# Performance work log

Measured on AMD Instinct MI355X. Metric: run time of the kernel, lower is better.

Reference implementation:

```python
import jax, jax.numpy as jnp
import numpy as np


def _cdist(x, y):
    # x: (b, n, c), y: (b, m, c) -> (b, n, m) Euclidean distances
    x2 = jnp.sum(x * x, axis=-1, keepdims=True)          # (b, n, 1)
    y2 = jnp.sum(y * y, axis=-1)[:, None, :]             # (b, 1, m)
    xy = jnp.einsum('bnc,bmc->bnm', x, y)                # (b, n, m)
    d2 = jnp.maximum(x2 + y2 - 2.0 * xy, 0.0)
    return jnp.sqrt(d2)


def setup_inputs() -> dict:
    key = jax.random.key(0)
    k1, k2, k3, k4 = jax.random.split(key, 4)
    bs, N, M, C = 8, 4096, 4096, 128
    return {
        'set1': jax.random.normal(k1, (bs, N, C), dtype=jnp.float32),
        'set2': jax.random.normal(k2, (bs, M, C), dtype=jnp.float32),
        'w1': jax.random.uniform(k3, (bs, N), dtype=jnp.float32),
        'w2': jax.random.uniform(k4, (bs, M), dtype=jnp.float32),
    }


def reference(set1, set2, w1, w2):
    dist = _cdist(set1, set2)                 # (b, N, M)
    out_dist = jnp.min(dist, axis=2)          # (b, N)
    out_dist2 = jnp.min(dist, axis=1)         # (b, M)
    total = (jnp.sum(w1 * out_dist) + jnp.sum(w2 * out_dist2)) / 2.0
    return total
```

## Files before the change

### kernel.cpp

```cpp
#include <hip/hip_runtime.h>

#define BS 8
#define NN 4096
#define MM 4096
#define CC 128
#define XT 128
#define YT 64
#define MH 2048
#define NYT (MH / YT)
#define NXT (NN / XT)

#define FINF_BITS 0x7F800000u

typedef __attribute__((ext_vector_type(8))) short bf16x8;
typedef __attribute__((ext_vector_type(4))) float f32x4;

__device__ inline ushort f2bf(float f) {
    unsigned u = __float_as_uint(f);
    unsigned r = (u + 0x7FFFu + ((u >> 16) & 1u)) >> 16;
    return (ushort)r;
}

__global__ void ch_prep(const float* __restrict__ y,
                        ushort* __restrict__ y16, float* __restrict__ yn,
                        unsigned* __restrict__ rowmin, unsigned* __restrict__ colmin,
                        float* __restrict__ out) {
    int gid = blockIdx.x * blockDim.x + threadIdx.x;
    size_t i = (size_t)gid * 4;

    float4 w = *(const float4*)(y + i);
    ushort4 p;
    p.x = f2bf(w.x); p.y = f2bf(w.y); p.z = f2bf(w.z); p.w = f2bf(w.w);
    *(ushort4*)(y16 + i) = p;
    float sy = w.x * w.x + w.y * w.y + w.z * w.z + w.w * w.w;

#pragma unroll
    for (int mask = 1; mask <= 16; mask <<= 1)
        sy += __shfl_xor(sy, mask, 64);
    if ((threadIdx.x & 31) == 0)
        yn[gid >> 5] = sy;

    if (gid < BS * NN) rowmin[gid] = FINF_BITS;
    if (gid < BS * MM) colmin[gid] = FINF_BITS;
    if (gid == 0) out[0] = 0.0f;
}

__global__ __launch_bounds__(256) void ch_tile(
    const float* __restrict__ Xf, const ushort* __restrict__ Y,
    const float* __restrict__ yn,
    unsigned* __restrict__ rowmin, unsigned* __restrict__ colmin) {

    __shared__ ushort xs[XT * CC];
    __shared__ ushort ys[2][YT * CC];
    __shared__ unsigned coltile[MH];
    __shared__ unsigned rowtile[XT];
    __shared__ float xnorm[XT];

    const int b  = blockIdx.x;
    const int xt = blockIdx.y;
    const int mh = blockIdx.z;
    const int n0 = xt * XT;
    const int m0 = mh * MH;
    const int tid  = threadIdx.x;
    const int wave = tid >> 6;
    const int lane = tid & 63;
    const int lc   = lane & 15;
    const int quad = lane >> 4;
    const int wm = wave >> 1;
    const int wn = wave & 1;

    const ushort* Yb = Y + ((size_t)b * MM + m0) * CC;

    const float* Xb = Xf + ((size_t)b * NN + n0) * CC;
    {
        float psum[8];
#pragma unroll
        for (int s = 0; s < 8; ++s) {
            int flat = s * 256 + tid;
            int r = flat >> 4, c = flat & 15;
            float4 v0 = *(const float4*)(Xb + (size_t)r * CC + c * 8);
            float4 v1 = *(const float4*)(Xb + (size_t)r * CC + c * 8 + 4);
            ushort h[8] = {f2bf(v0.x), f2bf(v0.y), f2bf(v0.z), f2bf(v0.w),
                           f2bf(v1.x), f2bf(v1.y), f2bf(v1.z), f2bf(v1.w)};
            *(bf16x8*)(xs + r * CC + (c ^ (r & 7)) * 8) = *(bf16x8*)h;
            psum[s] = v0.x * v0.x + v0.y * v0.y + v0.z * v0.z + v0.w * v0.w +
                      v1.x * v1.x + v1.y * v1.y + v1.z * v1.z + v1.w * v1.w;
        }
#pragma unroll
        for (int mask = 1; mask <= 8; mask <<= 1)
#pragma unroll
            for (int s = 0; s < 8; ++s)
                psum[s] += __shfl_xor(psum[s], mask, 64);
        if ((tid & 15) == 0) {
#pragma unroll
            for (int s = 0; s < 8; ++s)
                xnorm[s * 16 + (tid >> 4)] = psum[s];
        }
    }
    for (int c2 = tid; c2 < MH; c2 += 256) coltile[c2] = FINF_BITS;
    if (tid < XT) rowtile[tid] = FINF_BITS;

#pragma unroll
    for (int s = 0; s < 4; ++s) {
        int f = s * 256 + tid;
        int r = f >> 4, c = f & 15;
        const ushort* g = Yb + (size_t)r * CC + (c ^ (r & 15)) * 8;
        ushort* l = ys[0] + (s * 256 + wave * 64) * 8;
        __builtin_amdgcn_global_load_lds(
            (const __attribute__((address_space(1))) void*)g,
            (__attribute__((address_space(3))) void*)l, 16, 0, 0);
    }

    __syncthreads();

    float xnp[4][4];
#pragma unroll
    for (int i = 0; i < 4; ++i) {
        float4 t = *(const float4*)(&xnorm[wm * 64 + i * 16 + quad * 4]);
        xnp[i][0] = t.x; xnp[i][1] = t.y; xnp[i][2] = t.z; xnp[i][3] = t.w;
    }
    float rm[4][4];
#pragma unroll
    for (int i = 0; i < 4; ++i)
#pragma unroll
        for (int r = 0; r < 4; ++r) rm[i][r] = __builtin_inff();

    const float* ynb = yn + (size_t)b * MM + m0;
    const int xrow = (wm * 64 + lc) * CC;
    const int yrow = (wn * 32 + lc) * CC;
    const int xsw  = lc & 7;

#pragma unroll 1
    for (int mt = 0; mt < NYT; ++mt) {
        if (mt) __syncthreads();

        if (mt + 1 < NYT) {
            const ushort* Ysrc = Yb + (size_t)(mt + 1) * YT * CC;
            ushort* dstb = ys[(mt + 1) & 1];
#pragma unroll
            for (int s = 0; s < 4; ++s) {
                int f = s * 256 + tid;
                int r = f >> 4, c = f & 15;
                const ushort* g = Ysrc + (size_t)r * CC + (c ^ (r & 15)) * 8;
                ushort* l = dstb + (s * 256 + wave * 64) * 8;
                __builtin_amdgcn_global_load_lds(
                    (const __attribute__((address_space(1))) void*)g,
                    (__attribute__((address_space(3))) void*)l, 16, 0, 0);
            }
        }

        const ushort* yl = ys[mt & 1];

        float ynr[2];
#pragma unroll
        for (int j = 0; j < 2; ++j)
            ynr[j] = ynb[mt * YT + wn * 32 + j * 16 + lc];

        f32x4 acc[4][2];
        const f32x4 z = {0.f, 0.f, 0.f, 0.f};
#pragma unroll
        for (int kt = 0; kt < 4; ++kt) {
            bf16x8 af[4], yf[2];
            const int cx = ((kt * 4 + quad) ^ xsw) * 8;
            const int cy = ((kt * 4 + quad) ^ lc) * 8;
#pragma unroll
            for (int j = 0; j < 2; ++j)
                yf[j] = *(const bf16x8*)(yl + yrow + j * 16 * CC + cy);
#pragma unroll
            for (int i = 0; i < 4; ++i)
                af[i] = *(const bf16x8*)(xs + xrow + i * 16 * CC + cx);
#pragma unroll
            for (int j = 0; j < 2; ++j)
#pragma unroll
                for (int i = 0; i < 4; ++i)
                    acc[i][j] = __builtin_amdgcn_mfma_f32_16x16x32_bf16(
                        af[i], yf[j], (kt == 0) ? z : acc[i][j], 0, 0, 0);
        }

        float cmv[2];
#pragma unroll
        for (int j = 0; j < 2; ++j) cmv[j] = __builtin_inff();

#pragma unroll
        for (int i = 0; i < 4; ++i) {
#pragma unroll
            for (int j = 0; j < 2; ++j) {
                f32x4 a = acc[i][j];
#pragma unroll
                for (int r = 0; r < 4; ++r) {
                    float d2 = xnp[i][r] + fmaf(-2.0f, a[r], ynr[j]);
                    rm[i][r] = fminf(rm[i][r], d2);
                    cmv[j]   = fminf(cmv[j], d2);
                }
            }
        }

#pragma unroll
        for (int mask = 16; mask <= 32; mask <<= 1)
#pragma unroll
            for (int j = 0; j < 2; ++j)
                cmv[j] = fminf(cmv[j], __shfl_xor(cmv[j], mask, 64));
        if (quad == 0) {
#pragma unroll
            for (int j = 0; j < 2; ++j)
                atomicMin(&coltile[mt * YT + wn * 32 + j * 16 + lc],
                          __float_as_uint(fmaxf(cmv[j], 0.0f)));
        }
    }

#pragma unroll
    for (int mask = 1; mask <= 8; mask <<= 1)
#pragma unroll
        for (int i = 0; i < 4; ++i)
#pragma unroll
            for (int r = 0; r < 4; ++r)
                rm[i][r] = fminf(rm[i][r], __shfl_xor(rm[i][r], mask, 64));
    if (lc == 0) {
#pragma unroll
        for (int i = 0; i < 4; ++i)
#pragma unroll
            for (int r = 0; r < 4; ++r)
                atomicMin(&rowtile[wm * 64 + i * 16 + quad * 4 + r],
                          __float_as_uint(fmaxf(rm[i][r], 0.0f)));
    }

    __syncthreads();
    if (tid < XT)
        atomicMin(&rowmin[(size_t)b * NN + n0 + tid], rowtile[tid]);
    for (int c2 = tid; c2 < MH; c2 += 256)
        atomicMin(&colmin[(size_t)b * MM + m0 + c2], coltile[c2]);
}

__global__ void ch_finalize(const unsigned* __restrict__ rowmin,
                            const unsigned* __restrict__ colmin,
                            const float* __restrict__ w1,
                            const float* __restrict__ w2,
                            float* __restrict__ out) {
    int i = blockIdx.x * blockDim.x + threadIdx.x;
    int stride = gridDim.x * blockDim.x;
    float s = 0.f;
    for (int idx = i; idx < BS * NN; idx += stride)
        s += w1[idx] * sqrtf(__uint_as_float(rowmin[idx])) +
             w2[idx] * sqrtf(__uint_as_float(colmin[idx]));
#pragma unroll
    for (int off = 32; off > 0; off >>= 1) s += __shfl_down(s, off, 64);
    __shared__ float ls[4];
    int lane = threadIdx.x & 63, wv = threadIdx.x >> 6;
    if (lane == 0) ls[wv] = s;
    __syncthreads();
    if (threadIdx.x == 0) {
        float t = ls[0] + ls[1] + ls[2] + ls[3];
        atomicAdd(out, 0.5f * t);
    }
}

extern "C" void kernel_launch(void* const* d_in, const int* in_sizes, int n_in,
                              void* d_out, int out_size, void* d_ws, size_t ws_size,
                              hipStream_t stream) {
    const float* set1 = (const float*)d_in[0];
    const float* set2 = (const float*)d_in[1];
    const float* w1   = (const float*)d_in[2];
    const float* w2   = (const float*)d_in[3];
    float* out = (float*)d_out;

    ushort*   y16    = (ushort*)d_ws;
    float*    yn     = (float*)(y16 + (size_t)BS * MM * CC);
    unsigned* rowmin = (unsigned*)(yn + BS * MM);
    unsigned* colmin = rowmin + BS * NN;

    ch_prep<<<BS * MM * CC / 4 / 256, 256, 0, stream>>>(
        set2, y16, yn, rowmin, colmin, out);

    dim3 grid(BS, NXT, MM / MH);
    ch_tile<<<grid, 256, 0, stream>>>(set1, y16, yn, rowmin, colmin);

    ch_finalize<<<64, 256, 0, stream>>>(rowmin, colmin, w1, w2, out);
}
```

Baseline: 130.9 us.

## Enlarge Y tile to 128 rows staged in K-halves with 4x4 MFMA blocking

Doubles the Y tile per iteration to 128 rows. Each wave now computes a 64x64 output block with 16 accumulators instead of 8, which raises MFMA work per X-fragment LDS load. The Y tile is staged through LDS in two 64-channel halves, keeping the double buffer at its old size while pipelining across halves. The trade-offs are higher accumulator register pressure, twice as many barriers per tile, and a changed swizzle for the half-width buffer.

```diff
diff --git a/kernel.cpp b/kernel.cpp
--- a/kernel.cpp
+++ b/kernel.cpp
@@ -5,9 +5,9 @@
 #define MM 4096
 #define CC 128
 #define XT 128
-#define YT 64
+#define YT 128
 #define MH 2048
-#define NYT (MH / YT)
+#define NMT (MH / YT)
 #define NXT (NN / XT)
 
 #define FINF_BITS 0x7F800000u
@@ -45,13 +45,29 @@
     if (gid == 0) out[0] = 0.0f;
 }
 
+__device__ __forceinline__ void stage_y(const ushort* __restrict__ Yb,
+                                        ushort* __restrict__ buf,
+                                        int tile, int half, int tid, int wave) {
+#pragma unroll
+    for (int s = 0; s < 4; ++s) {
+        int f = s * 256 + tid;
+        int r = f >> 3, cslot = f & 7;
+        const ushort* g = Yb + (size_t)(tile * YT + r) * CC + half * 64 +
+                          ((cslot ^ (r & 7)) * 8);
+        ushort* l = buf + (size_t)(s * 256 + wave * 64) * 8;
+        __builtin_amdgcn_global_load_lds(
+            (const __attribute__((address_space(1))) void*)g,
+            (__attribute__((address_space(3))) void*)l, 16, 0, 0);
+    }
+}
+
 __global__ __launch_bounds__(256) void ch_tile(
     const float* __restrict__ Xf, const ushort* __restrict__ Y,
     const float* __restrict__ yn,
     unsigned* __restrict__ rowmin, unsigned* __restrict__ colmin) {
 
     __shared__ ushort xs[XT * CC];
-    __shared__ ushort ys[2][YT * CC];
+    __shared__ ushort ys[2][YT * 64];
     __shared__ unsigned coltile[MH];
     __shared__ unsigned rowtile[XT];
     __shared__ float xnorm[XT];
@@ -100,16 +116,7 @@
     for (int c2 = tid; c2 < MH; c2 += 256) coltile[c2] = FINF_BITS;
     if (tid < XT) rowtile[tid] = FINF_BITS;
 
-#pragma unroll
-    for (int s = 0; s < 4; ++s) {
-        int f = s * 256 + tid;
-        int r = f >> 4, c = f & 15;
-        const ushort* g = Yb + (size_t)r * CC + (c ^ (r & 15)) * 8;
-        ushort* l = ys[0] + (s * 256 + wave * 64) * 8;
-        __builtin_amdgcn_global_load_lds(
-            (const __attribute__((address_space(1))) void*)g,
-            (__attribute__((address_space(3))) void*)l, 16, 0, 0);
-    }
+    stage_y(Yb, ys[0], 0, 0, tid, wave);
 
     __syncthreads();
 
@@ -127,64 +134,59 @@
 
     const float* ynb = yn + (size_t)b * MM + m0;
     const int xrow = (wm * 64 + lc) * CC;
-    const int yrow = (wn * 32 + lc) * CC;
     const int xsw  = lc & 7;
 
 #pragma unroll 1
-    for (int mt = 0; mt < NYT; ++mt) {
-        if (mt) __syncthreads();
-
-        if (mt + 1 < NYT) {
-            const ushort* Ysrc = Yb + (size_t)(mt + 1) * YT * CC;
-            ushort* dstb = ys[(mt + 1) & 1];
-#pragma unroll
-            for (int s = 0; s < 4; ++s) {
-                int f = s * 256 + tid;
-                int r = f >> 4, c = f & 15;
-                const ushort* g = Ysrc + (size_t)r * CC + (c ^ (r & 15)) * 8;
-                ushort* l = dstb + (s * 256 + wave * 64) * 8;
-                __builtin_amdgcn_global_load_lds(
-                    (const __attribute__((address_space(1))) void*)g,
-                    (__attribute__((address_space(3))) void*)l, 16, 0, 0);
+    for (int t = 0; t < NMT; ++t) {
+        float ynr[4];
+        f32x4 acc[4][4];
+        const f32x4 z = {0.f, 0.f, 0.f, 0.f};
+
+#pragma unroll
+        for (int h = 0; h < 2; ++h) {
+            const int p = (2 * t + h) & 1;
+            if (t + h) __syncthreads();
+
+            const int nh = 2 * t + h + 1;
+            if (nh < 2 * NMT)
+                stage_y(Yb, ys[p ^ 1], nh >> 1, nh & 1, tid, wave);
+
+            if (h == 0) {
+#pragma unroll
+                for (int j = 0; j < 4; ++j)
+                    ynr[j] = ynb[t * YT + wn * 64 + j * 16 + lc];
             }
-        }
-
-        const ushort* yl = ys[mt & 1];
-
-        float ynr[2];
-#pragma unroll
-        for (int j = 0; j < 2; ++j)
-            ynr[j] = ynb[mt * YT + wn * 32 + j * 16 + lc];
-
-        f32x4 acc[4][2];
-        const f32x4 z = {0.f, 0.f, 0.f, 0.f};
-#pragma unroll
-        for (int kt = 0; kt < 4; ++kt) {
-            bf16x8 af[4], yf[2];
-            const int cx = ((kt * 4 + quad) ^ xsw) * 8;
-            const int cy = ((kt * 4 + quad) ^ lc) * 8;
-#pragma unroll
-            for (int j = 0; j < 2; ++j)
-                yf[j] = *(const bf16x8*)(yl + yrow + j * 16 * CC + cy);
-#pragma unroll
-            for (int i = 0; i < 4; ++i)
-                af[i] = *(const bf16x8*)(xs + xrow + i * 16 * CC + cx);
-#pragma unroll
-            for (int j = 0; j < 2; ++j)
+
+            const ushort* yl = ys[p];
+#pragma unroll
+            for (int s2 = 0; s2 < 2; ++s2) {
+                const int ktg = h * 2 + s2;
+                bf16x8 af[4], yf[4];
+                const int cx = ((ktg * 4 + quad) ^ xsw) * 8;
+                const int cy = ((s2 * 4 + quad) ^ xsw) * 8;
+#pragma unroll
+                for (int j = 0; j < 4; ++j)
+                    yf[j] = *(const bf16x8*)(yl + (wn * 64 + j * 16 + lc) * 64 + cy);
 #pragma unroll
                 for (int i = 0; i < 4; ++i)
-                    acc[i][j] = __builtin_amdgcn_mfma_f32_16x16x32_bf16(
-                        af[i], yf[j], (kt == 0) ? z : acc[i][j], 0, 0, 0);
-        }
-
-        float cmv[2];
-#pragma unroll
-        for (int j = 0; j < 2; ++j) cmv[j] = __builtin_inff();
+                    af[i] = *(const bf16x8*)(xs + xrow + i * 16 * CC + cx);
+#pragma unroll
+                for (int j = 0; j < 4; ++j)
+#pragma unroll
+                    for (int i = 0; i < 4; ++i)
+                        acc[i][j] = __builtin_amdgcn_mfma_f32_16x16x32_bf16(
+                            af[i], yf[j], (ktg == 0) ? z : acc[i][j], 0, 0, 0);
+            }
+        }
+
+        float cmv[4];
+#pragma unroll
+        for (int j = 0; j < 4; ++j) cmv[j] = __builtin_inff();
 
 #pragma unroll
         for (int i = 0; i < 4; ++i) {
 #pragma unroll
-            for (int j = 0; j < 2; ++j) {
+            for (int j = 0; j < 4; ++j) {
                 f32x4 a = acc[i][j];
 #pragma unroll
                 for (int r = 0; r < 4; ++r) {
@@ -198,12 +200,12 @@
 #pragma unroll
         for (int mask = 16; mask <= 32; mask <<= 1)
 #pragma unroll
-            for (int j = 0; j < 2; ++j)
+            for (int j = 0; j < 4; ++j)
                 cmv[j] = fminf(cmv[j], __shfl_xor(cmv[j], mask, 64));
         if (quad == 0) {
 #pragma unroll
-            for (int j = 0; j < 2; ++j)
-                atomicMin(&coltile[mt * YT + wn * 32 + j * 16 + lc],
+            for (int j = 0; j < 4; ++j)
+                atomicMin(&coltile[t * YT + wn * 64 + j * 16 + lc],
                           __float_as_uint(fmaxf(cmv[j], 0.0f)));
         }
     }
```

After: 128.0 us. 1.02x faster.
